# Kernel tuning notes

Hardware: AMD Instinct MI355X
Metric: run time of the kernel (lower is better)

## Reference

```python
import jax, jax.numpy as jnp
import numpy as np

N, D, H = 8192, 1024, 256

def setup_inputs() -> dict:
    key = jax.random.key(0)
    ks = jax.random.split(key, 11)
    s = lambda fan_in: 1.0 / np.sqrt(fan_in)
    return {
        "x": jax.random.normal(ks[0], (N, D), dtype=jnp.float32),
        "lin1_w": jax.random.uniform(ks[1], (H, D), jnp.float32, -s(D), s(D)),
        "lin1_b": jax.random.uniform(ks[2], (H,), jnp.float32, -s(D), s(D)),
        "q_w": jax.random.uniform(ks[3], (H, H), jnp.float32, -s(H), s(H)),
        "q_b": jax.random.uniform(ks[4], (H,), jnp.float32, -s(H), s(H)),
        "k_w": jax.random.uniform(ks[5], (H, H), jnp.float32, -s(H), s(H)),
        "k_b": jax.random.uniform(ks[6], (H,), jnp.float32, -s(H), s(H)),
        "v_w": jax.random.uniform(ks[7], (H, H), jnp.float32, -s(H), s(H)),
        "v_b": jax.random.uniform(ks[8], (H,), jnp.float32, -s(H), s(H)),
        "lin2_w": jax.random.uniform(ks[9], (1, H), jnp.float32, -s(H), s(H)),
        "lin2_b": jax.random.uniform(ks[10], (1,), jnp.float32, -s(H), s(H)),
    }

def reference(x, lin1_w, lin1_b, q_w, q_b, k_w, k_b, v_w, v_b, lin2_w, lin2_b):
    h = x @ lin1_w.T + lin1_b                      # [N, H]
    q = h @ q_w.T + q_b                            # [N, H]
    k = h @ k_w.T + k_b                            # [N, H]
    v = h @ v_w.T + v_b                            # [N, H]
    scale = 1.0 / np.sqrt(H).astype(np.float32)
    w = (q @ k.T) * scale                          # [N, N] dense scores
    a = jax.nn.softmax(w, axis=-1)                 # row softmax
    h = h + a @ v                                  # residual
    out = h @ lin2_w.T + lin2_b                    # [N, 1]
    return out.squeeze(-1)                         # [N]
```

## Files before the change

### kernel.cpp

```cpp
#include <hip/hip_runtime.h>
#include <hip/hip_bf16.h>
#include <math.h>

typedef __attribute__((ext_vector_type(4))) float f32x4;
typedef __attribute__((ext_vector_type(8))) short bf16x8;

#define N_TOK 8192
#define D_IN  1024
#define H_DIM 256
#define S_SPLIT 16
#define QSCALE 0.09016844f

static __device__ __forceinline__ float bf2f(unsigned short u) {
  return __uint_as_float(((unsigned)u) << 16);
}
static __device__ __forceinline__ float fast_exp2(float x) {
  float e;
  asm("v_exp_f32 %0, %1" : "=v"(e) : "v"(x));
  return e;
}
static __device__ __forceinline__ void gload_lds16(const void* g, void* l) {
  __builtin_amdgcn_global_load_lds(
      (const __attribute__((address_space(1))) void*)g,
      (__attribute__((address_space(3))) void*)l, 16, 0, 0);
}
#define QLOAD(dst, base, off) \
  asm volatile("global_load_dwordx4 %0, %1, off offset:" #off \
               : "=v"(dst) : "v"(base))

__global__ __launch_bounds__(256) void prep_kernel(
    const float* __restrict__ w1, const float* __restrict__ qw,
    const float* __restrict__ kw, const float* __restrict__ vw,
    const float* __restrict__ vb, const float* __restrict__ w2,
    __hip_bfloat16* __restrict__ w1b, __hip_bfloat16* __restrict__ qwb,
    __hip_bfloat16* __restrict__ kwb, float* __restrict__ wv2, float* __restrict__ bv2)
{
  int b = blockIdx.x, tid = threadIdx.x;
  if (b < 384) {
    const float* in; __hip_bfloat16* out; int base;
    if (b < 256)      { in = w1; out = w1b; base = b; }
    else if (b < 320) { in = qw; out = qwb; base = b - 256; }
    else              { in = kw; out = kwb; base = b - 320; }
    int i = base * 1024 + tid * 4;
    float4 v = *reinterpret_cast<const float4*>(in + i);
    union { __hip_bfloat16 h[4]; ushort4 u; } cv;
    cv.h[0] = __float2bfloat16(v.x);
    cv.h[1] = __float2bfloat16(v.y);
    cv.h[2] = __float2bfloat16(v.z);
    cv.h[3] = __float2bfloat16(v.w);
    *reinterpret_cast<ushort4*>(out + i) = cv.u;
    return;
  }
  __shared__ float sw2[256];
  __shared__ __attribute__((aligned(16))) float vch[32 * 256];
  sw2[tid] = w2[tid];
  float a = 0.f;
  for (int ch = 0; ch < 8; ++ch) {
    __syncthreads();
    #pragma unroll
    for (int i = 0; i < 8; ++i) {
      int p = i * 1024 + tid * 4;
      *reinterpret_cast<float4*>(vch + p) =
          *reinterpret_cast<const float4*>(vw + ch * 8192 + p);
    }
    __syncthreads();
    #pragma unroll
    for (int c = 0; c < 32; ++c)
      a = fmaf(vch[c * 256 + tid], sw2[ch * 32 + c], a);
  }
  wv2[tid] = a;
  __syncthreads();
  vch[tid] = vb[tid] * sw2[tid];
  __syncthreads();
  for (int s = 128; s > 0; s >>= 1) {
    if (tid < s) vch[tid] += vch[tid + s];
    __syncthreads();
  }
  if (tid == 0) bv2[0] = vch[0];
}

__global__ __launch_bounds__(512) void front_kernel(
    const float* __restrict__ x, const __hip_bfloat16* __restrict__ W1,
    const __hip_bfloat16* __restrict__ Wq, const __hip_bfloat16* __restrict__ Wk,
    const float* __restrict__ b1, const float* __restrict__ bq, const float* __restrict__ bk,
    const float* __restrict__ w2, const float* __restrict__ wv2, const float* __restrict__ b2,
    __hip_bfloat16* __restrict__ Qo, __hip_bfloat16* __restrict__ Ko,
    float* __restrict__ hw2, float* __restrict__ vs)
{
  __shared__ __attribute__((aligned(16))) unsigned char h_lds[16384];
  __shared__ __attribute__((aligned(16))) unsigned char sbuf[2][36864];
  const int tid = threadIdx.x;
  const int w = tid >> 6, l = tid & 63, r16 = l & 15, kg = l >> 4;
  const int wr = w >> 2, wc = w & 3;
  const int rowbase = blockIdx.x * 32;
  const int rsw = (r16 & 7) << 4;

  const int xrow = tid >> 4, xc = tid & 15;
  const float* xsrc = x + (size_t)(rowbase + xrow) * D_IN + xc * 4;
  const int xdst = xrow * 128 + ((xc * 8) ^ ((xrow & 7) << 4));
  const char* W1b = (const char*)W1;

  f32x4 acc[4];
  #pragma unroll
  for (int c = 0; c < 4; ++c) acc[c] = (f32x4){0.f, 0.f, 0.f, 0.f};

  {
    f32x4 xv = *reinterpret_cast<const f32x4*>(xsrc);
    #pragma unroll
    for (int i = 0; i < 4; ++i) {
      int p = i * 8192 + tid * 16;
      int col = p >> 7, bb = p & 127;
      gload_lds16(W1b + (size_t)col * 2048 + (bb ^ ((col & 7) << 4)), &sbuf[0][4096 + p]);
    }
    union { __hip_bfloat16 h[4]; ushort4 u; } cv;
    cv.h[0] = __float2bfloat16(xv[0]); cv.h[1] = __float2bfloat16(xv[1]);
    cv.h[2] = __float2bfloat16(xv[2]); cv.h[3] = __float2bfloat16(xv[3]);
    *reinterpret_cast<ushort4*>(&sbuf[0][xdst]) = cv.u;
  }
  __syncthreads();

  for (int t = 0; t < 16; ++t) {
    const int cur = t & 1;
    f32x4 xv;
    if (t + 1 < 16) {
      xv = *reinterpret_cast<const f32x4*>(xsrc + (t + 1) * 64);
      const int k0b = (t + 1) * 128;
      #pragma unroll
      for (int i = 0; i < 4; ++i) {
        int p = i * 8192 + tid * 16;
        int col = p >> 7, bb = p & 127;
        gload_lds16(W1b + (size_t)col * 2048 + k0b + (bb ^ ((col & 7) << 4)),
                    &sbuf[cur ^ 1][4096 + p]);
      }
    }
    const unsigned char* A = &sbuf[cur][0];
    const unsigned char* W = &sbuf[cur][4096];
    #pragma unroll
    for (int ks = 0; ks < 2; ++ks) {
      bf16x8 a = *reinterpret_cast<const bf16x8*>(
          A + (wr * 16 + r16) * 128 + ((ks * 64 + kg * 16) ^ rsw));
      #pragma unroll
      for (int c = 0; c < 4; ++c) {
        const int colloc = wc * 64 + c * 16 + r16;
        bf16x8 b = *reinterpret_cast<const bf16x8*>(
            W + colloc * 128 + ((ks * 64 + kg * 16) ^ rsw));
        acc[c] = __builtin_amdgcn_mfma_f32_16x16x32_bf16(a, b, acc[c], 0, 0, 0);
      }
    }
    if (t + 1 < 16) {
      union { __hip_bfloat16 h[4]; ushort4 u; } cv;
      cv.h[0] = __float2bfloat16(xv[0]); cv.h[1] = __float2bfloat16(xv[1]);
      cv.h[2] = __float2bfloat16(xv[2]); cv.h[3] = __float2bfloat16(xv[3]);
      *reinterpret_cast<ushort4*>(&sbuf[cur ^ 1][xdst]) = cv.u;
    }
    __syncthreads();
  }

  #pragma unroll
  for (int c = 0; c < 4; ++c) {
    int col = wc * 64 + c * 16 + r16;
    float bs = b1[col];
    #pragma unroll
    for (int j = 0; j < 4; ++j) {
      int row = wr * 16 + kg * 4 + j;
      *reinterpret_cast<__hip_bfloat16*>(
          &h_lds[row * 512 + ((col * 2) ^ ((row & 7) << 4))]) =
          __float2bfloat16(acc[c][j] + bs);
    }
  }

  const char* wqB = (const char*)Wq;
  const char* wkB = (const char*)Wk;
  #pragma unroll
  for (int i = 0; i < 4; ++i) {
    int p = i * 8192 + tid * 16;
    int col = p >> 7, bb = p & 127;
    gload_lds16(wqB + (size_t)col * 512 + (bb ^ ((col & 7) << 4)), &sbuf[0][p]);
  }
  __syncthreads();

  f32x4 qacc[4];
  #pragma unroll
  for (int c = 0; c < 4; ++c) qacc[c] = (f32x4){0.f, 0.f, 0.f, 0.f};

  for (int r = 0; r < 8; ++r) {
    const int buf = r & 1;
    if (r + 1 < 8) {
      const char* Wsel = (r + 1 < 4) ? wqB : wkB;
      const int kq1 = (r + 1) & 3;
      #pragma unroll
      for (int i = 0; i < 4; ++i) {
        int p = i * 8192 + tid * 16;
        int col = p >> 7, bb = p & 127;
        gload_lds16(Wsel + (size_t)col * 512 + kq1 * 128 + (bb ^ ((col & 7) << 4)),
                    &sbuf[buf ^ 1][p]);
      }
    }
    const int kq = r & 3;
    const unsigned char* WT = &sbuf[buf][0];
    #pragma unroll
    for (int ks = 0; ks < 2; ++ks) {
      bf16x8 a = *reinterpret_cast<const bf16x8*>(
          &h_lds[(wr * 16 + r16) * 512 + ((kq * 128 + ks * 64 + kg * 16) ^ rsw)]);
      #pragma unroll
      for (int c = 0; c < 4; ++c) {
        const int colloc = wc * 64 + c * 16 + r16;
        bf16x8 b = *reinterpret_cast<const bf16x8*>(
            WT + colloc * 128 + ((ks * 64 + kg * 16) ^ rsw));
        qacc[c] = __builtin_amdgcn_mfma_f32_16x16x32_bf16(a, b, qacc[c], 0, 0, 0);
      }
    }
    if (r == 3) {
      #pragma unroll
      for (int c = 0; c < 4; ++c) {
        int col = wc * 64 + c * 16 + r16;
        float bb = bq[col];
        #pragma unroll
        for (int j = 0; j < 4; ++j) {
          int row = rowbase + wr * 16 + kg * 4 + j;
          Qo[(size_t)row * H_DIM + col] = __float2bfloat16((qacc[c][j] + bb) * QSCALE);
        }
        qacc[c] = (f32x4){0.f, 0.f, 0.f, 0.f};
      }
    }
    __syncthreads();
  }
  #pragma unroll
  for (int c = 0; c < 4; ++c) {
    int col = wc * 64 + c * 16 + r16;
    float bb = bk[col];
    #pragma unroll
    for (int j = 0; j < 4; ++j) {
      int row = rowbase + wr * 16 + kg * 4 + j;
      Ko[(size_t)row * H_DIM + col] = __float2bfloat16(qacc[c][j] + bb);
    }
  }

  {
    const bool isw2 = (w < 4);
    const float* wsel = isw2 ? w2 : wv2;
    const int c16 = l & 15;
    #pragma unroll
    for (int pass = 0; pass < 2; ++pass) {
      int row = (w & 3) * 8 + pass * 4 + (l >> 4);
      int rs2 = (row & 7) << 4;
      bf16x8 h0 = *reinterpret_cast<const bf16x8*>(&h_lds[row * 512 + ((c16 * 32) ^ rs2)]);
      bf16x8 h1 = *reinterpret_cast<const bf16x8*>(&h_lds[row * 512 + ((c16 * 32 + 16) ^ rs2)]);
      float s = 0.f;
      #pragma unroll
      for (int i = 0; i < 8; ++i) s += bf2f((unsigned short)h0[i]) * wsel[c16 * 16 + i];
      #pragma unroll
      for (int i = 0; i < 8; ++i) s += bf2f((unsigned short)h1[i]) * wsel[c16 * 16 + 8 + i];
      #pragma unroll
      for (int off = 1; off < 16; off <<= 1) s += __shfl_xor(s, off);
      if (c16 == 0) {
        if (isw2) hw2[rowbase + row] = s + b2[0];
        else      vs[rowbase + row]  = s;
      }
    }
  }
}

#define KVBLK 64
#define KRANGE (N_TOK / S_SPLIT)
__global__ __launch_bounds__(256, 2) void attn_partial_kernel(
    const __hip_bfloat16* __restrict__ Q, const __hip_bfloat16* __restrict__ K,
    const float* __restrict__ vsg, float* __restrict__ pden, float* __restrict__ pacc)
{
  __shared__ __attribute__((aligned(16))) unsigned char ktile[2][KVBLK * 512];
  __shared__ float vs_lds[KRANGE];

  const int tid = threadIdx.x;
  const int w   = tid >> 6;
  const int l   = tid & 63;
  const int r16 = l & 15;
  const int kg  = l >> 4;
  const int split   = blockIdx.y;
  const int mstart  = split * KRANGE;
  const int rowbase = blockIdx.x * 256 + w * 64;

  if (tid < KRANGE / 4)
    *reinterpret_cast<float4*>(vs_lds + tid * 4) =
        *reinterpret_cast<const float4*>(vsg + mstart + tid * 4);

  bf16x8 qf[4][8];
  #pragma unroll
  for (int sub = 0; sub < 4; ++sub) {
    const char* qp = (const char*)(Q + (size_t)(rowbase + sub * 16 + r16) * H_DIM + kg * 8);
    QLOAD(qf[sub][0], qp, 0);
    QLOAD(qf[sub][1], qp, 64);
    QLOAD(qf[sub][2], qp, 128);
    QLOAD(qf[sub][3], qp, 192);
    QLOAD(qf[sub][4], qp, 256);
    QLOAD(qf[sub][5], qp, 320);
    QLOAD(qf[sub][6], qp, 384);
    QLOAD(qf[sub][7], qp, 448);
  }
  asm volatile("s_waitcnt vmcnt(0)" ::: "memory");

  const int trow = tid >> 5;
  const int tbsw = ((tid & 31) * 16) ^ ((trow & 7) << 4);
  const char* kbase = (const char*)K + (size_t)(mstart + trow) * 512 + tbsw;
  const int ldst = trow * 512 + (tid & 31) * 16;

  const int rsw = (r16 & 7) << 4;
  const int cb  = kg * 16;

  float den[4][4], acc[4][4];
  #pragma unroll
  for (int sub = 0; sub < 4; ++sub)
    #pragma unroll
    for (int j = 0; j < 4; ++j) { den[sub][j] = 0.f; acc[sub][j] = 0.f; }

  #pragma unroll
  for (int i = 0; i < 8; ++i)
    gload_lds16(kbase + (size_t)(i * 8) * 512, &ktile[0][i * 4096 + ldst]);
  __syncthreads();

  const int NT = KRANGE / KVBLK;
  for (int t = 0; t < NT; ++t) {
    const int cur = t & 1;
    if (t + 1 < NT) {
      #pragma unroll
      for (int i = 0; i < 8; ++i)
        gload_lds16(kbase + (size_t)((t + 1) * KVBLK + i * 8) * 512,
                    &ktile[cur ^ 1][i * 4096 + ldst]);
    }

    const unsigned char* kt = &ktile[cur][0];
    #pragma unroll
    for (int h = 0; h < 2; ++h) {
      f32x4 d[4][2];
      #pragma unroll
      for (int sub = 0; sub < 4; ++sub)
        #pragma unroll
        for (int n = 0; n < 2; ++n) d[sub][n] = (f32x4){0.f, 0.f, 0.f, 0.f};

      __builtin_amdgcn_s_setprio(1);
      #pragma unroll
      for (int n = 0; n < 2; ++n) {
        const int row = h * 32 + n * 16 + r16;
        #pragma unroll
        for (int kk = 0; kk < 8; ++kk) {
          bf16x8 b = *reinterpret_cast<const bf16x8*>(
              kt + row * 512 + ((kk * 64 + cb) ^ rsw));
          d[0][n] = __builtin_amdgcn_mfma_f32_16x16x32_bf16(qf[0][kk], b, d[0][n], 0, 0, 0);
          d[1][n] = __builtin_amdgcn_mfma_f32_16x16x32_bf16(qf[1][kk], b, d[1][n], 0, 0, 0);
          d[2][n] = __builtin_amdgcn_mfma_f32_16x16x32_bf16(qf[2][kk], b, d[2][n], 0, 0, 0);
          d[3][n] = __builtin_amdgcn_mfma_f32_16x16x32_bf16(qf[3][kk], b, d[3][n], 0, 0, 0);
        }
      }
      __builtin_amdgcn_s_setprio(0);

      const float vsm0 = vs_lds[t * KVBLK + h * 32 + r16];
      const float vsm1 = vs_lds[t * KVBLK + h * 32 + 16 + r16];
      #pragma unroll
      for (int sub = 0; sub < 4; ++sub)
        #pragma unroll
        for (int j = 0; j < 4; ++j) {
          float e0 = fast_exp2(d[sub][0][j]);
          float e1 = fast_exp2(d[sub][1][j]);
          den[sub][j] += e0 + e1;
          acc[sub][j] = fmaf(e0, vsm0, fmaf(e1, vsm1, acc[sub][j]));
        }
    }
    __syncthreads();
  }

  #pragma unroll
  for (int sub = 0; sub < 4; ++sub)
    #pragma unroll
    for (int j = 0; j < 4; ++j) {
      #pragma unroll
      for (int off = 1; off < 16; off <<= 1) {
        den[sub][j] += __shfl_xor(den[sub][j], off);
        acc[sub][j] += __shfl_xor(acc[sub][j], off);
      }
    }
  if (r16 == 0) {
    #pragma unroll
    for (int sub = 0; sub < 4; ++sub)
      #pragma unroll
      for (int j = 0; j < 4; ++j) {
        int row = rowbase + sub * 16 + kg * 4 + j;
        pden[split * N_TOK + row] = den[sub][j];
        pacc[split * N_TOK + row] = acc[sub][j];
      }
  }
}

__global__ __launch_bounds__(256) void combine_kernel(
    const float* __restrict__ pden, const float* __restrict__ pacc,
    const float* __restrict__ hw2, const float* __restrict__ bv2, float* __restrict__ out)
{
  int r = blockIdx.x * 256 + threadIdx.x;
  float den = 0.f, acc = 0.f;
  #pragma unroll
  for (int s = 0; s < S_SPLIT; ++s) {
    den += pden[s * N_TOK + r];
    acc += pacc[s * N_TOK + r];
  }
  out[r] = hw2[r] + acc / den + bv2[0];
}

extern "C" void kernel_launch(void* const* d_in, const int* in_sizes, int n_in,
                              void* d_out, int out_size, void* d_ws, size_t ws_size,
                              hipStream_t stream) {
  const float* x      = (const float*)d_in[0];
  const float* lin1_w = (const float*)d_in[1];
  const float* lin1_b = (const float*)d_in[2];
  const float* q_w    = (const float*)d_in[3];
  const float* q_b    = (const float*)d_in[4];
  const float* k_w    = (const float*)d_in[5];
  const float* k_b    = (const float*)d_in[6];
  const float* v_w    = (const float*)d_in[7];
  const float* v_b    = (const float*)d_in[8];
  const float* lin2_w = (const float*)d_in[9];
  const float* lin2_b = (const float*)d_in[10];
  float* out = (float*)d_out;

  char* ws = (char*)d_ws;
  size_t off = 0;
  auto alloc = [&](size_t bytes) {
    char* p = ws + off;
    off += (bytes + 255) & ~(size_t)255;
    return p;
  };
  __hip_bfloat16* w1b = (__hip_bfloat16*)alloc((size_t)H_DIM * D_IN * 2);
  __hip_bfloat16* qwb = (__hip_bfloat16*)alloc((size_t)H_DIM * H_DIM * 2);
  __hip_bfloat16* kwb = (__hip_bfloat16*)alloc((size_t)H_DIM * H_DIM * 2);
  __hip_bfloat16* qb  = (__hip_bfloat16*)alloc((size_t)N_TOK * H_DIM * 2);
  __hip_bfloat16* kb  = (__hip_bfloat16*)alloc((size_t)N_TOK * H_DIM * 2);
  float* hw2  = (float*)alloc((size_t)N_TOK * 4);
  float* vsv  = (float*)alloc((size_t)N_TOK * 4);
  float* wv2  = (float*)alloc((size_t)H_DIM * 4);
  float* bv2  = (float*)alloc(256);
  float* pden = (float*)alloc((size_t)S_SPLIT * N_TOK * 4);
  float* pacc = (float*)alloc((size_t)S_SPLIT * N_TOK * 4);
  (void)ws_size; (void)in_sizes; (void)n_in; (void)out_size;

  prep_kernel<<<385, 256, 0, stream>>>(lin1_w, q_w, k_w, v_w, v_b, lin2_w,
                                       w1b, qwb, kwb, wv2, bv2);

  front_kernel<<<256, 512, 0, stream>>>(x, w1b, qwb, kwb, lin1_b, q_b, k_b,
                                        lin2_w, wv2, lin2_b, qb, kb, hw2, vsv);

  attn_partial_kernel<<<dim3(32, S_SPLIT), 256, 0, stream>>>(qb, kb, vsv, pden, pacc);

  combine_kernel<<<N_TOK / 256, 256, 0, stream>>>(pden, pacc, hw2, bv2, out);
}
```

Baseline: 82.46 us.

## Halve front-kernel row tile and parallelize v-weight folding in prep kernel

The front kernel now handles 16 rows per block instead of 32, doubling the grid to 512 blocks. It preloads the whole 16x1024 x tile into LDS as bf16 up front and streams W1 in 64-wide K chunks, with each wave owning 32 output columns. The prep kernel's serial single-block w_v·w2 reduction is spread across 8 blocks plus a separate bias-reduction block. The aim is better CU occupancy and a shorter prep critical path, at the cost of reading W1 and Wq/Wk twice as often overall and using more LDS per block.

```diff
diff --git a/kernel.cpp b/kernel.cpp
--- a/kernel.cpp
+++ b/kernel.cpp
@@ -51,32 +51,35 @@
     *reinterpret_cast<ushort4*>(out + i) = cv.u;
     return;
   }
-  __shared__ float sw2[256];
-  __shared__ __attribute__((aligned(16))) float vch[32 * 256];
-  sw2[tid] = w2[tid];
-  float a = 0.f;
-  for (int ch = 0; ch < 8; ++ch) {
-    __syncthreads();
-    #pragma unroll
-    for (int i = 0; i < 8; ++i) {
-      int p = i * 1024 + tid * 4;
-      *reinterpret_cast<float4*>(vch + p) =
-          *reinterpret_cast<const float4*>(vw + ch * 8192 + p);
-    }
-    __syncthreads();
-    #pragma unroll
-    for (int c = 0; c < 32; ++c)
-      a = fmaf(vch[c * 256 + tid], sw2[ch * 32 + c], a);
-  }
-  wv2[tid] = a;
-  __syncthreads();
-  vch[tid] = vb[tid] * sw2[tid];
+  if (b < 392) {
+    __shared__ float sw2b[256];
+    __shared__ float red2[8][32];
+    sw2b[tid] = w2[tid];
+    __syncthreads();
+    const int jb = (b - 384) * 32;
+    const int jj = tid & 31, cg = tid >> 5;
+    float a = 0.f;
+    #pragma unroll 8
+    for (int c = cg * 32; c < cg * 32 + 32; ++c)
+      a = fmaf(vw[c * 256 + jb + jj], sw2b[c], a);
+    red2[cg][jj] = a;
+    __syncthreads();
+    if (tid < 32) {
+      float s = 0.f;
+      #pragma unroll
+      for (int g = 0; g < 8; ++g) s += red2[g][tid];
+      wv2[jb + tid] = s;
+    }
+    return;
+  }
+  __shared__ float red[256];
+  red[tid] = vb[tid] * w2[tid];
   __syncthreads();
   for (int s = 128; s > 0; s >>= 1) {
-    if (tid < s) vch[tid] += vch[tid + s];
-    __syncthreads();
-  }
-  if (tid == 0) bv2[0] = vch[0];
+    if (tid < s) red[tid] += red[tid + s];
+    __syncthreads();
+  }
+  if (tid == 0) bv2[0] = red[0];
 }
 
 __global__ __launch_bounds__(512) void front_kernel(
@@ -87,84 +90,77 @@
     __hip_bfloat16* __restrict__ Qo, __hip_bfloat16* __restrict__ Ko,
     float* __restrict__ hw2, float* __restrict__ vs)
 {
-  __shared__ __attribute__((aligned(16))) unsigned char h_lds[16384];
-  __shared__ __attribute__((aligned(16))) unsigned char sbuf[2][36864];
+  __shared__ __attribute__((aligned(16))) unsigned char lds[73728];
   const int tid = threadIdx.x;
   const int w = tid >> 6, l = tid & 63, r16 = l & 15, kg = l >> 4;
-  const int wr = w >> 2, wc = w & 3;
-  const int rowbase = blockIdx.x * 32;
-  const int rsw = (r16 & 7) << 4;
-
-  const int xrow = tid >> 4, xc = tid & 15;
-  const float* xsrc = x + (size_t)(rowbase + xrow) * D_IN + xc * 4;
-  const int xdst = xrow * 128 + ((xc * 8) ^ ((xrow & 7) << 4));
+  const int rowbase = blockIdx.x * 16;
+  const int rsw8 = (r16 & 7) << 4;
   const char* W1b = (const char*)W1;
 
-  f32x4 acc[4];
-  #pragma unroll
-  for (int c = 0; c < 4; ++c) acc[c] = (f32x4){0.f, 0.f, 0.f, 0.f};
-
   {
-    f32x4 xv = *reinterpret_cast<const f32x4*>(xsrc);
+    const int xrow = tid >> 5;
+    const int xcb  = (tid & 31) * 64;
+    const float* xp = x + (size_t)(rowbase + xrow) * D_IN + (tid & 31) * 32;
+    f32x4 xr[8];
+    #pragma unroll
+    for (int i = 0; i < 8; ++i) xr[i] = *reinterpret_cast<const f32x4*>(xp + i * 4);
     #pragma unroll
     for (int i = 0; i < 4; ++i) {
-      int p = i * 8192 + tid * 16;
-      int col = p >> 7, bb = p & 127;
-      gload_lds16(W1b + (size_t)col * 2048 + (bb ^ ((col & 7) << 4)), &sbuf[0][4096 + p]);
-    }
-    union { __hip_bfloat16 h[4]; ushort4 u; } cv;
-    cv.h[0] = __float2bfloat16(xv[0]); cv.h[1] = __float2bfloat16(xv[1]);
-    cv.h[2] = __float2bfloat16(xv[2]); cv.h[3] = __float2bfloat16(xv[3]);
-    *reinterpret_cast<ushort4*>(&sbuf[0][xdst]) = cv.u;
+      union { __hip_bfloat16 h[8]; uint4 u; } cv;
+      #pragma unroll
+      for (int e = 0; e < 4; ++e) {
+        cv.h[e]     = __float2bfloat16(xr[2 * i][e]);
+        cv.h[4 + e] = __float2bfloat16(xr[2 * i + 1][e]);
+      }
+      *reinterpret_cast<uint4*>(&lds[xrow * 2048 + ((xcb + i * 16) ^ ((xrow & 7) << 4))]) = cv.u;
+    }
+  }
+
+  f32x4 acc[2];
+  acc[0] = (f32x4){0.f, 0.f, 0.f, 0.f};
+  acc[1] = (f32x4){0.f, 0.f, 0.f, 0.f};
+
+  #pragma unroll
+  for (int i = 0; i < 2; ++i) {
+    int p = i * 8192 + tid * 16;
+    int col = p >> 6, bb = p & 63;
+    gload_lds16(W1b + (size_t)col * 2048 + (bb ^ ((col & 3) << 4)), &lds[32768 + p]);
   }
   __syncthreads();
 
-  for (int t = 0; t < 16; ++t) {
+  for (int t = 0; t < 32; ++t) {
     const int cur = t & 1;
-    f32x4 xv;
-    if (t + 1 < 16) {
-      xv = *reinterpret_cast<const f32x4*>(xsrc + (t + 1) * 64);
-      const int k0b = (t + 1) * 128;
-      #pragma unroll
-      for (int i = 0; i < 4; ++i) {
+    if (t + 1 < 32) {
+      #pragma unroll
+      for (int i = 0; i < 2; ++i) {
         int p = i * 8192 + tid * 16;
-        int col = p >> 7, bb = p & 127;
-        gload_lds16(W1b + (size_t)col * 2048 + k0b + (bb ^ ((col & 7) << 4)),
-                    &sbuf[cur ^ 1][4096 + p]);
-      }
-    }
-    const unsigned char* A = &sbuf[cur][0];
-    const unsigned char* W = &sbuf[cur][4096];
-    #pragma unroll
-    for (int ks = 0; ks < 2; ++ks) {
-      bf16x8 a = *reinterpret_cast<const bf16x8*>(
-          A + (wr * 16 + r16) * 128 + ((ks * 64 + kg * 16) ^ rsw));
-      #pragma unroll
-      for (int c = 0; c < 4; ++c) {
-        const int colloc = wc * 64 + c * 16 + r16;
-        bf16x8 b = *reinterpret_cast<const bf16x8*>(
-            W + colloc * 128 + ((ks * 64 + kg * 16) ^ rsw));
-        acc[c] = __builtin_amdgcn_mfma_f32_16x16x32_bf16(a, b, acc[c], 0, 0, 0);
-      }
-    }
-    if (t + 1 < 16) {
-      union { __hip_bfloat16 h[4]; ushort4 u; } cv;
-      cv.h[0] = __float2bfloat16(xv[0]); cv.h[1] = __float2bfloat16(xv[1]);
-      cv.h[2] = __float2bfloat16(xv[2]); cv.h[3] = __float2bfloat16(xv[3]);
-      *reinterpret_cast<ushort4*>(&sbuf[cur ^ 1][xdst]) = cv.u;
-    }
-    __syncthreads();
-  }
-
-  #pragma unroll
-  for (int c = 0; c < 4; ++c) {
-    int col = wc * 64 + c * 16 + r16;
+        int col = p >> 6, bb = p & 63;
+        gload_lds16(W1b + (size_t)col * 2048 + (t + 1) * 64 + (bb ^ ((col & 3) << 4)),
+                    &lds[32768 + (cur ^ 1) * 16384 + p]);
+      }
+    }
+    const unsigned char* Wc = &lds[32768 + cur * 16384];
+    bf16x8 a = *reinterpret_cast<const bf16x8*>(
+        &lds[r16 * 2048 + ((t * 64 + kg * 16) ^ rsw8)]);
+    #pragma unroll
+    for (int c = 0; c < 2; ++c) {
+      const int colloc = w * 32 + c * 16 + r16;
+      bf16x8 b = *reinterpret_cast<const bf16x8*>(
+          Wc + colloc * 64 + ((kg * 16) ^ ((colloc & 3) << 4)));
+      acc[c] = __builtin_amdgcn_mfma_f32_16x16x32_bf16(a, b, acc[c], 0, 0, 0);
+    }
+    __syncthreads();
+  }
+
+  #pragma unroll
+  for (int c = 0; c < 2; ++c) {
+    int col = w * 32 + c * 16 + r16;
     float bs = b1[col];
     #pragma unroll
     for (int j = 0; j < 4; ++j) {
-      int row = wr * 16 + kg * 4 + j;
+      int row = kg * 4 + j;
       *reinterpret_cast<__hip_bfloat16*>(
-          &h_lds[row * 512 + ((col * 2) ^ ((row & 7) << 4))]) =
+          &lds[65536 + row * 512 + ((col * 2) ^ ((row & 7) << 4))]) =
           __float2bfloat16(acc[c][j] + bs);
     }
   }
@@ -175,16 +171,16 @@
   for (int i = 0; i < 4; ++i) {
     int p = i * 8192 + tid * 16;
     int col = p >> 7, bb = p & 127;
-    gload_lds16(wqB + (size_t)col * 512 + (bb ^ ((col & 7) << 4)), &sbuf[0][p]);
+    gload_lds16(wqB + (size_t)col * 512 + (bb ^ ((col & 7) << 4)), &lds[p]);
   }
   __syncthreads();
 
-  f32x4 qacc[4];
-  #pragma unroll
-  for (int c = 0; c < 4; ++c) qacc[c] = (f32x4){0.f, 0.f, 0.f, 0.f};
+  f32x4 qacc[2];
+  qacc[0] = (f32x4){0.f, 0.f, 0.f, 0.f};
+  qacc[1] = (f32x4){0.f, 0.f, 0.f, 0.f};
 
   for (int r = 0; r < 8; ++r) {
-    const int buf = r & 1;
+    const int bufoff = (r & 1) ? 32768 : 0;
     if (r + 1 < 8) {
       const char* Wsel = (r + 1 < 4) ? wqB : wkB;
       const int kq1 = (r + 1) & 3;
@@ -193,31 +189,31 @@
         int p = i * 8192 + tid * 16;
         int col = p >> 7, bb = p & 127;
         gload_lds16(Wsel + (size_t)col * 512 + kq1 * 128 + (bb ^ ((col & 7) << 4)),
-                    &sbuf[buf ^ 1][p]);
+                    &lds[(bufoff ^ 32768) + p]);
       }
     }
     const int kq = r & 3;
-    const unsigned char* WT = &sbuf[buf][0];
+    const unsigned char* WT = &lds[bufoff];
     #pragma unroll
     for (int ks = 0; ks < 2; ++ks) {
       bf16x8 a = *reinterpret_cast<const bf16x8*>(
-          &h_lds[(wr * 16 + r16) * 512 + ((kq * 128 + ks * 64 + kg * 16) ^ rsw)]);
-      #pragma unroll
-      for (int c = 0; c < 4; ++c) {
-        const int colloc = wc * 64 + c * 16 + r16;
+          &lds[65536 + r16 * 512 + ((kq * 128 + ks * 64 + kg * 16) ^ rsw8)]);
+      #pragma unroll
+      for (int c = 0; c < 2; ++c) {
+        const int colloc = w * 32 + c * 16 + r16;
         bf16x8 b = *reinterpret_cast<const bf16x8*>(
-            WT + colloc * 128 + ((ks * 64 + kg * 16) ^ rsw));
+            WT + colloc * 128 + ((ks * 64 + kg * 16) ^ ((colloc & 7) << 4)));
         qacc[c] = __builtin_amdgcn_mfma_f32_16x16x32_bf16(a, b, qacc[c], 0, 0, 0);
       }
     }
     if (r == 3) {
       #pragma unroll
-      for (int c = 0; c < 4; ++c) {
-        int col = wc * 64 + c * 16 + r16;
+      for (int c = 0; c < 2; ++c) {
+        int col = w * 32 + c * 16 + r16;
         float bb = bq[col];
         #pragma unroll
         for (int j = 0; j < 4; ++j) {
-          int row = rowbase + wr * 16 + kg * 4 + j;
+          int row = rowbase + kg * 4 + j;
           Qo[(size_t)row * H_DIM + col] = __float2bfloat16((qacc[c][j] + bb) * QSCALE);
         }
         qacc[c] = (f32x4){0.f, 0.f, 0.f, 0.f};
@@ -226,12 +222,12 @@
     __syncthreads();
   }
   #pragma unroll
-  for (int c = 0; c < 4; ++c) {
-    int col = wc * 64 + c * 16 + r16;
+  for (int c = 0; c < 2; ++c) {
+    int col = w * 32 + c * 16 + r16;
     float bb = bk[col];
     #pragma unroll
     for (int j = 0; j < 4; ++j) {
-      int row = rowbase + wr * 16 + kg * 4 + j;
+      int row = rowbase + kg * 4 + j;
       Ko[(size_t)row * H_DIM + col] = __float2bfloat16(qacc[c][j] + bb);
     }
   }
@@ -240,23 +236,20 @@
     const bool isw2 = (w < 4);
     const float* wsel = isw2 ? w2 : wv2;
     const int c16 = l & 15;
-    #pragma unroll
-    for (int pass = 0; pass < 2; ++pass) {
-      int row = (w & 3) * 8 + pass * 4 + (l >> 4);
-      int rs2 = (row & 7) << 4;
-      bf16x8 h0 = *reinterpret_cast<const bf16x8*>(&h_lds[row * 512 + ((c16 * 32) ^ rs2)]);
-      bf16x8 h1 = *reinterpret_cast<const bf16x8*>(&h_lds[row * 512 + ((c16 * 32 + 16) ^ rs2)]);
-      float s = 0.f;
-      #pragma unroll
-      for (int i = 0; i < 8; ++i) s += bf2f((unsigned short)h0[i]) * wsel[c16 * 16 + i];
-      #pragma unroll
-      for (int i = 0; i < 8; ++i) s += bf2f((unsigned short)h1[i]) * wsel[c16 * 16 + 8 + i];
-      #pragma unroll
-      for (int off = 1; off < 16; off <<= 1) s += __shfl_xor(s, off);
-      if (c16 == 0) {
-        if (isw2) hw2[rowbase + row] = s + b2[0];
-        else      vs[rowbase + row]  = s;
-      }
+    const int row = (w & 3) * 4 + (l >> 4);
+    const int rs2 = (row & 7) << 4;
+    bf16x8 h0 = *reinterpret_cast<const bf16x8*>(&lds[65536 + row * 512 + ((c16 * 32) ^ rs2)]);
+    bf16x8 h1 = *reinterpret_cast<const bf16x8*>(&lds[65536 + row * 512 + ((c16 * 32 + 16) ^ rs2)]);
+    float s = 0.f;
+    #pragma unroll
+    for (int i = 0; i < 8; ++i) s += bf2f((unsigned short)h0[i]) * wsel[c16 * 16 + i];
+    #pragma unroll
+    for (int i = 0; i < 8; ++i) s += bf2f((unsigned short)h1[i]) * wsel[c16 * 16 + 8 + i];
+    #pragma unroll
+    for (int off = 1; off < 16; off <<= 1) s += __shfl_xor(s, off);
+    if (c16 == 0) {
+      if (isw2) hw2[rowbase + row] = s + b2[0];
+      else      vs[rowbase + row]  = s;
     }
   }
 }
@@ -439,11 +432,11 @@
   float* pacc = (float*)alloc((size_t)S_SPLIT * N_TOK * 4);
   (void)ws_size; (void)in_sizes; (void)n_in; (void)out_size;
 
-  prep_kernel<<<385, 256, 0, stream>>>(lin1_w, q_w, k_w, v_w, v_b, lin2_w,
+  prep_kernel<<<393, 256, 0, stream>>>(lin1_w, q_w, k_w, v_w, v_b, lin2_w,
                                        w1b, qwb, kwb, wv2, bv2);
 
-  front_kernel<<<256, 512, 0, stream>>>(x, w1b, qwb, kwb, lin1_b, q_b, k_b,
-                                        lin2_w, wv2, lin2_b, qb, kb, hw2, vsv);
+  front_kernel<<<N_TOK / 16, 512, 0, stream>>>(x, w1b, qwb, kwb, lin1_b, q_b, k_b,
+                                               lin2_w, wv2, lin2_b, qb, kb, hw2, vsv);
 
   attn_partial_kernel<<<dim3(32, S_SPLIT), 256, 0, stream>>>(qb, kb, vsv, pden, pacc);
 
```

Result: no change. 82.07 us (-0.5%).
